# Kernel optimization log

Hardware: AMD Instinct MI355X
Metric: run time of the kernel (lower is better)

The kernel has to match this reference:

```python
import jax, jax.numpy as jnp
import numpy as np

N = 50000      # num nodes
E = 1600000    # num edges
C = 128        # channels
F = 4          # number of framelet filters
K = 6          # Chebyshev order
S = 1.0        # spectral scale s
APPROX = np.array([[0.3, 0.15, 0.1, 0.075, 0.06, 0.05],
                   [0.6, 0.3, 0.2, 0.15, 0.12, 0.1],
                   [0.9, 0.45, 0.3, 0.225, 0.18, 0.15],
                   [1.2, 0.6, 0.4, 0.3, 0.24, 0.2]], dtype=np.float32)


def setup_inputs() -> dict:
    key = jax.random.key(0)
    ks = jax.random.split(key, 6)
    scale = (2.0 / C) ** 0.5
    return {
        "x_real": jax.random.normal(ks[0], (N, C), jnp.float32),
        "x_imag": jax.random.normal(ks[1], (N, C), jnp.float32),
        "edge_index": jax.random.randint(ks[2], (2, E), 0, N, dtype=jnp.int32),
        "edge_weight": jax.random.uniform(ks[3], (E,), jnp.float32),
        "approx": jnp.asarray(APPROX),
        "theta": jnp.ones((F,), jnp.float32),
        "W_r": jax.random.normal(ks[4], (C, C), jnp.float32) * scale,
        "W_i": jax.random.normal(ks[5], (C, C), jnp.float32) * scale,
        "num_nodes": N,
    }


def _framelet_fwd(x_real, x_imag, edge_index, edge_weight, approx, theta, W_r, W_i, num_nodes):
    row, col = edge_index[0], edge_index[1]
    w = edge_weight / S

    def A_norm(h):  # h: [N, C] real; normalized adjacency propagation
        return jax.ops.segment_sum(w[:, None] * h[col], row, num_segments=num_nodes)

    # Linearity: sum_i theta_i * sum_k approx[i,k] * T_k(x) == sum_k c_k * T_k(x)
    c = theta @ approx  # [K] effective Chebyshev coefficients

    T0r, T0i = x_real, x_imag
    out_r = c[0] * T0r
    out_i = c[0] * T0i
    T1r, T1i = -A_norm(T0r), -A_norm(T0i)
    out_r = out_r + c[1] * T1r
    out_i = out_i + c[1] * T1i
    for ki in range(2, K):
        T2r = -2.0 * A_norm(T1r) - T0r
        T2i = -2.0 * A_norm(T1i) - T0i
        out_r = out_r + c[ki] * T2r
        out_i = out_i + c[ki] * T2i
        T0r, T0i, T1r, T1i = T1r, T1i, T2r, T2i

    # complex linear: (r + i*j) @ (W_r + W_i*j)^T
    yr = out_r @ W_r.T - out_i @ W_i.T
    yi = out_r @ W_i.T + out_i @ W_r.T
    # CSiLU: SiLU applied to real/imag parts independently
    return jnp.stack([jax.nn.silu(yr), jax.nn.silu(yi)])  # [2, N, C]


def reference(x_real, x_imag, edge_index, edge_weight, approx, theta, W_r, W_i, num_nodes):
    return _framelet_fwd(x_real, x_imag, edge_index, edge_weight, approx, theta, W_r, W_i, num_nodes)
```

## Files before the change

kernel.cpp:

```cpp
#include <hip/hip_runtime.h>
#include <hip/hip_fp16.h>
#include <math.h>


#define CH   128
#define NP   128
#define NP4  64
#define RPB  128
#define MAXBUCK 512

typedef _Float16 half8 __attribute__((ext_vector_type(8)));
typedef float f32x4 __attribute__((ext_vector_type(4)));

__device__ __forceinline__ uint2 ntload_u2(const uint2* p) {
    unsigned long long v = __builtin_nontemporal_load((const unsigned long long*)p);
    uint2 r; r.x = (unsigned)v; r.y = (unsigned)(v >> 32);
    return r;
}


__global__ __launch_bounds__(256) void bucket_hist_k(
        const int* __restrict__ row, int* __restrict__ bucket_cnt, int E, int nbuck) {
    __shared__ int h[MAXBUCK];
    for (int j = threadIdx.x; j < nbuck; j += 256) h[j] = 0;
    __syncthreads();
    int stride = gridDim.x * 256;
    for (int e = blockIdx.x * 256 + threadIdx.x; e < E; e += stride)
        atomicAdd(&h[row[e] >> 7], 1);
    __syncthreads();
    for (int j = threadIdx.x; j < nbuck; j += 256)
        if (h[j]) atomicAdd(&bucket_cnt[j], h[j]);
}

__global__ __launch_bounds__(512) void bucket_scan_k(
        const int* __restrict__ bucket_cnt, int* __restrict__ bucket_start,
        int* __restrict__ bucket_cursor, int nbuck, int E) {
    __shared__ int sd[MAXBUCK];
    int t = threadIdx.x;
    int v = (t < nbuck) ? bucket_cnt[t] : 0;
    sd[t] = v;
    __syncthreads();
    for (int off = 1; off < MAXBUCK; off <<= 1) {
        int y = (t >= off) ? sd[t - off] : 0;
        __syncthreads();
        sd[t] += y;
        __syncthreads();
    }
    int excl = sd[t] - v;
    if (t < nbuck) { bucket_start[t] = excl; bucket_cursor[t] = excl; }
    if (t == 0) bucket_start[nbuck] = E;
}

__global__ __launch_bounds__(256) void bucket_place_k(
        const int* __restrict__ row, const int* __restrict__ col,
        const float* __restrict__ w, int* __restrict__ bucket_cursor,
        uint2* __restrict__ tmp, int E, int chunk, int nbuck) {
    __shared__ int cnt[MAXBUCK];
    __shared__ int cur[MAXBUCK];
    int e0 = blockIdx.x * chunk;
    int e1 = e0 + chunk; if (e1 > E) e1 = E;
    if (e0 >= E) return;
    for (int j = threadIdx.x; j < nbuck; j += 256) cnt[j] = 0;
    __syncthreads();
    for (int e = e0 + threadIdx.x; e < e1; e += 256)
        atomicAdd(&cnt[row[e] >> 7], 1);
    __syncthreads();
    for (int j = threadIdx.x; j < nbuck; j += 256) {
        int c = cnt[j];
        cur[j] = c ? atomicAdd(&bucket_cursor[j], c) : 0;
    }
    __syncthreads();
    for (int e = e0 + threadIdx.x; e < e1; e += 256) {
        int r = row[e];
        int b = r >> 7;
        int p = atomicAdd(&cur[b], 1);
        uint2 ent;
        ent.x = ((unsigned)(r & (RPB - 1)) << 16) | (unsigned)col[e];
        ent.y = __float_as_uint(w[e]);
        tmp[p] = ent;
    }
}

__global__ __launch_bounds__(256) void csr_build_k(
        const uint2* __restrict__ tmp, const int* __restrict__ bucket_start,
        int* __restrict__ row_start, unsigned* __restrict__ csr4,
        int N, int E, int nbuck) {
    __shared__ int hist[RPB];
    __shared__ int sc[RPB];
    __shared__ int curs[RPB];
    int b = blockIdx.x;
    int t = threadIdx.x;
    int base = bucket_start[b];
    int endp = bucket_start[b + 1];
    if (t < RPB) hist[t] = 0;
    __syncthreads();
    for (int e = base + t; e < endp; e += 256)
        atomicAdd(&hist[tmp[e].x >> 16], 1);
    __syncthreads();
    if (t < RPB) sc[t] = hist[t];
    __syncthreads();
    for (int off = 1; off < RPB; off <<= 1) {
        int y = 0;
        if (t < RPB && t >= off) y = sc[t - off];
        __syncthreads();
        if (t < RPB) sc[t] += y;
        __syncthreads();
    }
    int r0 = b << 7;
    if (t < RPB) {
        int excl = sc[t] - hist[t];
        if (r0 + t < N) row_start[r0 + t] = base + excl;
        curs[t] = base + excl;
    }
    if (b == nbuck - 1 && t == 0) row_start[N] = E;
    __syncthreads();
    for (int e = base + t; e < endp; e += 256) {
        uint2 ent = tmp[e];
        int rl = ent.x >> 16;
        unsigned c = ent.x & 0xffffu;
        float wv = __uint_as_float(ent.y) * (-1.0f / 16.0f);
        int p = atomicAdd(&curs[rl], 1);
        __half hw = __float2half(wv);
        csr4[p] = (c << 16) | (unsigned)__half_as_ushort(hw);
    }
}

__global__ void coef_k(const float* __restrict__ approx, const float* __restrict__ theta,
                       float* cp) {
    int k = threadIdx.x;
    if (k < 6 && blockIdx.x == 0) {
        float s = 0.f;
        for (int f = 0; f < 4; f++) s += theta[f] * approx[f * 6 + k];
        float sc = 1.f;
        for (int j = 0; j < k; j++) sc *= 32.f;
        cp[k] = s * sc;
    }
}

__global__ void convert_x_k(const float2* __restrict__ xr2, const float2* __restrict__ xi2,
                            __half2* __restrict__ xbuf, int total) {
    int idx = blockIdx.x * blockDim.x + threadIdx.x;
    if (idx >= total) return;
    int i = idx >> 7;
    int p = idx & 127;
    float2 v = (p < 64) ? xr2[(size_t)i * 64 + p] : xi2[(size_t)i * 64 + (p - 64)];
    xbuf[idx] = __floats2half2_rn(v.x, v.y);
}

__global__ void build_whT_k(const float* __restrict__ Wr, const float* __restrict__ Wi,
                            _Float16* __restrict__ WhT) {
    int idx = blockIdx.x * 256 + threadIdx.x;
    int j = idx >> 8, k = idx & 255;
    float v;
    if (j < 128) {
        v = (k < 128) ? Wr[j * 128 + k] : -Wi[j * 128 + (k - 128)];
    } else {
        v = (k < 128) ? Wi[(j - 128) * 128 + k] : Wr[(j - 128) * 128 + (k - 128)];
    }
    WhT[idx] = (_Float16)v;
}


__device__ __forceinline__ void unpack4(uint2 v, float& a, float& b, float& c, float& d) {
    __half2 lo = *reinterpret_cast<__half2*>(&v.x);
    __half2 hi = *reinterpret_cast<__half2*>(&v.y);
    float2 f0 = __half22float2(lo);
    float2 f1 = __half22float2(hi);
    a = f0.x; b = f0.y; c = f1.x; d = f1.y;
}

__device__ __forceinline__ void decode(unsigned ent, int& c, float& wv) {
    c = (int)(ent >> 16);
    wv = __half2float(__ushort_as_half((unsigned short)(ent & 0xffffu)));
}

__device__ __forceinline__ void gather_row(
        const uint2* __restrict__ src, const unsigned* __restrict__ csr,
        int beg, int end, int p4,
        float& s0, float& s1, float& s2, float& s3) {
    int e = beg;
    unsigned c0, c1, c2, c3;
    if (e + 4 <= end) { c0 = csr[e]; c1 = csr[e+1]; c2 = csr[e+2]; c3 = csr[e+3]; }
    for (; e + 8 <= end; e += 4) {
        unsigned n0 = csr[e+4], n1 = csr[e+5], n2 = csr[e+6], n3 = csr[e+7];
        int ia, ib, ic, id; float wa, wb, wc, wd;
        decode(c0, ia, wa); decode(c1, ib, wb); decode(c2, ic, wc); decode(c3, id, wd);
        float a0,a1,a2,a3, b0,b1,b2,b3, d0,d1,d2,d3, f0,f1,f2,f3;
        unpack4(src[(size_t)ia * NP4 + p4], a0,a1,a2,a3);
        unpack4(src[(size_t)ib * NP4 + p4], b0,b1,b2,b3);
        unpack4(src[(size_t)ic * NP4 + p4], d0,d1,d2,d3);
        unpack4(src[(size_t)id * NP4 + p4], f0,f1,f2,f3);
        s0 += wa*a0 + wb*b0 + wc*d0 + wd*f0;
        s1 += wa*a1 + wb*b1 + wc*d1 + wd*f1;
        s2 += wa*a2 + wb*b2 + wc*d2 + wd*f2;
        s3 += wa*a3 + wb*b3 + wc*d3 + wd*f3;
        c0 = n0; c1 = n1; c2 = n2; c3 = n3;
    }
    if (e + 4 <= end) {
        int ia, ib, ic, id; float wa, wb, wc, wd;
        decode(c0, ia, wa); decode(c1, ib, wb); decode(c2, ic, wc); decode(c3, id, wd);
        float a0,a1,a2,a3, b0,b1,b2,b3, d0,d1,d2,d3, f0,f1,f2,f3;
        unpack4(src[(size_t)ia * NP4 + p4], a0,a1,a2,a3);
        unpack4(src[(size_t)ib * NP4 + p4], b0,b1,b2,b3);
        unpack4(src[(size_t)ic * NP4 + p4], d0,d1,d2,d3);
        unpack4(src[(size_t)id * NP4 + p4], f0,f1,f2,f3);
        s0 += wa*a0 + wb*b0 + wc*d0 + wd*f0;
        s1 += wa*a1 + wb*b1 + wc*d1 + wd*f1;
        s2 += wa*a2 + wb*b2 + wc*d2 + wd*f2;
        s3 += wa*a3 + wb*b3 + wc*d3 + wd*f3;
        e += 4;
    }
    for (; e < end; e++) {
        int ia; float wa;
        decode(csr[e], ia, wa);
        float a0,a1,a2,a3;
        unpack4(src[(size_t)ia * NP4 + p4], a0,a1,a2,a3);
        s0 += wa*a0; s1 += wa*a1; s2 += wa*a2; s3 += wa*a3;
    }
}

__global__ __launch_bounds__(256) void spmm_first4_k(
        const uint2* __restrict__ xb4,
        const int* __restrict__ row_start, const unsigned* __restrict__ csr,
        uint2* __restrict__ dst, int N) {
    int t = threadIdx.x;
    int rl = t >> 6;
    int p4 = t & 63;
    int i = blockIdx.x * 4 + rl;
    if (i >= N) return;
    int beg = row_start[i], end = row_start[i + 1];
    float s0 = 0.f, s1 = 0.f, s2 = 0.f, s3 = 0.f;
    gather_row(xb4, csr, beg, end, p4, s0, s1, s2, s3);
    s0 *= 0.5f; s1 *= 0.5f; s2 *= 0.5f; s3 *= 0.5f;
    uint2 pk;
    __half2 h0 = __floats2half2_rn(s0, s1);
    __half2 h1 = __floats2half2_rn(s2, s3);
    pk.x = *reinterpret_cast<unsigned*>(&h0);
    pk.y = *reinterpret_cast<unsigned*>(&h1);
    dst[(size_t)i * NP4 + p4] = pk;
}

__global__ __launch_bounds__(256) void spmm_step4_k(
        const uint2* __restrict__ cur, const uint2* __restrict__ prev,
        const int* __restrict__ row_start, const unsigned* __restrict__ csr,
        uint2* __restrict__ dst, int N) {
    int t = threadIdx.x;
    int rl = t >> 6;
    int p4 = t & 63;
    int i = blockIdx.x * 4 + rl;
    if (i >= N) return;
    int beg = row_start[i], end = row_start[i + 1];
    float s0 = 0.f, s1 = 0.f, s2 = 0.f, s3 = 0.f;
    gather_row(cur, csr, beg, end, p4, s0, s1, s2, s3);
    float p0,p1,p2,p3;
    unpack4(ntload_u2(&prev[(size_t)i * NP4 + p4]), p0,p1,p2,p3);
    const float inv = 1.0f / 1024.0f;
    float t0 = s0 - inv * p0;
    float t1v = s1 - inv * p1;
    float t2v = s2 - inv * p2;
    float t3v = s3 - inv * p3;
    uint2 pk;
    __half2 h0 = __floats2half2_rn(t0, t1v);
    __half2 h1 = __floats2half2_rn(t2v, t3v);
    pk.x = *reinterpret_cast<unsigned*>(&h0);
    pk.y = *reinterpret_cast<unsigned*>(&h1);
    dst[(size_t)i * NP4 + p4] = pk;
}

__global__ __launch_bounds__(256) void gemm_silu_mfma_k(
        const _Float16* __restrict__ WhT,
        const uint2* __restrict__ x0, const uint2* __restrict__ t1b,
        const uint2* __restrict__ t2b, const uint2* __restrict__ t3b,
        const float* __restrict__ cp,
        float* __restrict__ out, int N) {
    __shared__ _Float16 U[32][264];
    int t = threadIdx.x;
    int row0 = blockIdx.x * 32;
    const uint2* t4b = (const uint2*)out;
    const uint2* t5b = (const uint2*)out + (size_t)N * NP4;
    const float isc = 1.0f / 32.0f;
    float w0 = cp[0], w1 = cp[1], w2 = cp[2], w3 = cp[3], w4 = cp[4], w5 = cp[5];
    for (int q = t; q < 2048; q += 256) {
        int r = q >> 6;
        int s = q & 63;
        int row = row0 + r;
        float a0 = 0.f, a1 = 0.f, a2 = 0.f, a3 = 0.f;
        if (row < N) {
            size_t idx = (size_t)row * NP4 + s;
            float v0,v1,v2,v3;
            unpack4(ntload_u2(&x0[idx]),  v0,v1,v2,v3);
            a0 += w0*v0; a1 += w0*v1; a2 += w0*v2; a3 += w0*v3;
            unpack4(ntload_u2(&t1b[idx]), v0,v1,v2,v3);
            a0 += w1*v0; a1 += w1*v1; a2 += w1*v2; a3 += w1*v3;
            unpack4(ntload_u2(&t2b[idx]), v0,v1,v2,v3);
            a0 += w2*v0; a1 += w2*v1; a2 += w2*v2; a3 += w2*v3;
            unpack4(ntload_u2(&t3b[idx]), v0,v1,v2,v3);
            a0 += w3*v0; a1 += w3*v1; a2 += w3*v2; a3 += w3*v3;
            unpack4(ntload_u2(&t4b[idx]), v0,v1,v2,v3);
            a0 += w4*v0; a1 += w4*v1; a2 += w4*v2; a3 += w4*v3;
            unpack4(ntload_u2(&t5b[idx]), v0,v1,v2,v3);
            a0 += w5*v0; a1 += w5*v1; a2 += w5*v2; a3 += w5*v3;
        }
        int k = s * 4;
        U[r][k]   = (_Float16)(a0 * isc);
        U[r][k+1] = (_Float16)(a1 * isc);
        U[r][k+2] = (_Float16)(a2 * isc);
        U[r][k+3] = (_Float16)(a3 * isc);
    }
    __syncthreads();

    int wave = t >> 6;
    int lane = t & 63;
    int colbase = wave * 64;
    int lr = lane & 15;
    int lg = lane >> 4;
    f32x4 acc[2][4] = {};
    for (int kb = 0; kb < 8; kb++) {
        int k0 = kb * 32 + lg * 8;
        half8 a0 = *(const half8*)&U[lr][k0];
        half8 a1 = *(const half8*)&U[16 + lr][k0];
        #pragma unroll
        for (int nf = 0; nf < 4; nf++) {
            int col = colbase + nf * 16 + lr;
            half8 b = *(const half8*)&WhT[(size_t)col * 256 + k0];
            acc[0][nf] = __builtin_amdgcn_mfma_f32_16x16x32_f16(a0, b, acc[0][nf], 0, 0, 0);
            acc[1][nf] = __builtin_amdgcn_mfma_f32_16x16x32_f16(a1, b, acc[1][nf], 0, 0, 0);
        }
    }

    #pragma unroll
    for (int mf = 0; mf < 2; mf++) {
        #pragma unroll
        for (int nf = 0; nf < 4; nf++) {
            int col = colbase + nf * 16 + lr;
            int half = col >> 7, j = col & 127;
            #pragma unroll
            for (int r4 = 0; r4 < 4; r4++) {
                int row = row0 + mf * 16 + lg * 4 + r4;
                if (row < N) {
                    float v = acc[mf][nf][r4] * 32.f;
                    float sv = v / (1.f + expf(-v));
                    out[(size_t)half * N * CH + (size_t)row * CH + j] = sv;
                }
            }
        }
    }
}


extern "C" void kernel_launch(void* const* d_in, const int* in_sizes, int n_in,
                              void* d_out, int out_size, void* d_ws, size_t ws_size,
                              hipStream_t stream) {
    const float* xr     = (const float*)d_in[0];
    const float* xi     = (const float*)d_in[1];
    const int*   eidx   = (const int*)d_in[2];
    const float* ew     = (const float*)d_in[3];
    const float* approx = (const float*)d_in[4];
    const float* theta  = (const float*)d_in[5];
    const float* Wr     = (const float*)d_in[6];
    const float* Wi     = (const float*)d_in[7];

    const int N = in_sizes[0] / CH;
    const int E = in_sizes[3];
    const int* rowv = eidx;
    const int* colv = eidx + E;

    float* outp = (float*)d_out;

    char* w8 = (char*)d_ws;
    size_t off = 0;
    auto alloc = [&](size_t bytes) -> void* {
        void* ptr = w8 + off;
        off += (bytes + 255) & ~(size_t)255;
        return ptr;
    };
    float*    cp        = (float*)alloc(64 * 4);
    int*      bucket_cnt= (int*)alloc(MAXBUCK * 4);
    int*      bucket_st = (int*)alloc((MAXBUCK + 1) * 4);
    int*      bucket_cur= (int*)alloc(MAXBUCK * 4);
    int*      row_start = (int*)alloc((size_t)(N + 1) * 4);
    unsigned* csr4      = (unsigned*)alloc((size_t)E * 4);
    _Float16* WhT       = (_Float16*)alloc(256 * 256 * 2);
    uint2*    xbuf      = (uint2*)alloc((size_t)N * NP4 * 8);
    uint2*    T1        = (uint2*)alloc((size_t)N * NP4 * 8);
    uint2*    T2        = (uint2*)alloc((size_t)N * NP4 * 8);
    uint2*    T3        = (uint2*)alloc((size_t)N * NP4 * 8);
    uint2*    tmp       = T3;
    uint2*    T4        = (uint2*)d_out;
    uint2*    T5        = (uint2*)d_out + (size_t)N * NP4;
    (void)ws_size;

    const int nbuck = (N + RPB - 1) / RPB;
    const int chunk = (E + 255) / 256;
    const int NH = N * NP;

    hipMemsetAsync(bucket_cnt, 0, (size_t)MAXBUCK * 4, stream);
    coef_k<<<1, 64, 0, stream>>>(approx, theta, cp);
    build_whT_k<<<256, 256, 0, stream>>>(Wr, Wi, WhT);
    bucket_hist_k<<<256, 256, 0, stream>>>(rowv, bucket_cnt, E, nbuck);
    bucket_scan_k<<<1, MAXBUCK, 0, stream>>>(bucket_cnt, bucket_st, bucket_cur, nbuck, E);
    bucket_place_k<<<256, 256, 0, stream>>>(rowv, colv, ew, bucket_cur, tmp, E, chunk, nbuck);
    csr_build_k<<<nbuck, 256, 0, stream>>>(tmp, bucket_st, row_start, csr4, N, E, nbuck);
    convert_x_k<<<(NH + 255) / 256, 256, 0, stream>>>(
        (const float2*)xr, (const float2*)xi, (__half2*)xbuf, NH);

    const int NG = (N + 3) / 4;

    spmm_first4_k<<<NG, 256, 0, stream>>>(xbuf, row_start, csr4, T1, N);
    spmm_step4_k<<<NG, 256, 0, stream>>>(T1, xbuf, row_start, csr4, T2, N);
    spmm_step4_k<<<NG, 256, 0, stream>>>(T2, T1, row_start, csr4, T3, N);
    spmm_step4_k<<<NG, 256, 0, stream>>>(T3, T2, row_start, csr4, T4, N);
    spmm_step4_k<<<NG, 256, 0, stream>>>(T4, T3, row_start, csr4, T5, N);

    gemm_silu_mfma_k<<<(N + 31) / 32, 256, 0, stream>>>(
        WhT, xbuf, T1, T2, T3, cp, outp, N);
}
```

Baseline: 658.8 us.

## Tile feature layout into 8-channel-chunk blocks and degree-sort row pairs for SpMM

Feature buffers now use a blocked layout in which each 8-row group stores 64-byte column chunks contiguously. The SpMM grid is split into 8 channel slices per block, so each gather touches a narrower slice that is more likely to stay in cache. Rows are processed in pairs sorted by max degree through a histogram, scan and scatter, which balances the per-wave work, and outputs use nontemporal stores. This adds three preprocessing kernels and sorted-index indirection. Because N/2 pairs only cover 2*(N/2) rows, an odd N would leave the last row unhandled.

Result: slower. 743.3 us (+12.8%).

```diff
diff --git a/kernel.cpp b/kernel.cpp
--- a/kernel.cpp
+++ b/kernel.cpp
@@ -4,8 +4,6 @@
 
 
 #define CH   128
-#define NP   128
-#define NP4  64
 #define RPB  128
 #define MAXBUCK 512
 
@@ -16,6 +14,14 @@
     unsigned long long v = __builtin_nontemporal_load((const unsigned long long*)p);
     uint2 r; r.x = (unsigned)v; r.y = (unsigned)(v >> 32);
     return r;
+}
+__device__ __forceinline__ void ntstore_u2(uint2* p, uint2 v) {
+    unsigned long long q = (unsigned long long)v.x | ((unsigned long long)v.y << 32);
+    __builtin_nontemporal_store(q, (unsigned long long*)p);
+}
+
+__device__ __forceinline__ size_t foff(int i, int cbase ) {
+    return ((size_t)((unsigned)i >> 3) << 9) + (((unsigned)i & 7u) << 3) + cbase;
 }
 
 
@@ -125,6 +131,54 @@
     }
 }
 
+
+__global__ __launch_bounds__(256) void pair_hist_k(
+        const int* __restrict__ row_start, int* __restrict__ ph, int NP_) {
+    __shared__ int h[256];
+    if (threadIdx.x < 256) h[threadIdx.x] = 0;
+    __syncthreads();
+    int stride = gridDim.x * 256;
+    for (int i = blockIdx.x * 256 + threadIdx.x; i < NP_; i += stride) {
+        int a = row_start[2*i], b = row_start[2*i+1], c = row_start[2*i+2];
+        int d = max(b - a, c - b);
+        if (d > 255) d = 255;
+        atomicAdd(&h[d], 1);
+    }
+    __syncthreads();
+    if (threadIdx.x < 256 && h[threadIdx.x]) atomicAdd(&ph[threadIdx.x], h[threadIdx.x]);
+}
+
+__global__ __launch_bounds__(256) void pair_scan_k(
+        const int* __restrict__ ph, int* __restrict__ pcur) {
+    __shared__ int sd[256];
+    int t = threadIdx.x;
+    int v = ph[t];
+    sd[t] = v;
+    __syncthreads();
+    for (int off = 1; off < 256; off <<= 1) {
+        int y = (t >= off) ? sd[t - off] : 0;
+        __syncthreads();
+        sd[t] += y;
+        __syncthreads();
+    }
+    pcur[t] = sd[t] - v;
+}
+
+__global__ __launch_bounds__(256) void pair_scatter_k(
+        const int* __restrict__ row_start, int* __restrict__ pcur,
+        int* __restrict__ sbeg, int* __restrict__ send, int* __restrict__ sorig,
+        int NP_) {
+    int i = blockIdx.x * 256 + threadIdx.x;
+    if (i >= NP_) return;
+    int a = row_start[2*i], b = row_start[2*i+1], c = row_start[2*i+2];
+    int d = max(b - a, c - b);
+    if (d > 255) d = 255;
+    int q = atomicAdd(&pcur[d], 1);
+    int p = 2 * q;
+    sbeg[p]   = a; send[p]   = b; sorig[p]   = 2*i;
+    sbeg[p+1] = b; send[p+1] = c; sorig[p+1] = 2*i + 1;
+}
+
 __global__ void coef_k(const float* __restrict__ approx, const float* __restrict__ theta,
                        float* cp) {
     int k = threadIdx.x;
@@ -137,14 +191,22 @@
     }
 }
 
-__global__ void convert_x_k(const float2* __restrict__ xr2, const float2* __restrict__ xi2,
-                            __half2* __restrict__ xbuf, int total) {
+__global__ void convert_x_k(const float4* __restrict__ xr4, const float4* __restrict__ xi4,
+                            uint2* __restrict__ xbuf, int N) {
     int idx = blockIdx.x * blockDim.x + threadIdx.x;
-    if (idx >= total) return;
-    int i = idx >> 7;
-    int p = idx & 127;
-    float2 v = (p < 64) ? xr2[(size_t)i * 64 + p] : xi2[(size_t)i * 64 + (p - 64)];
-    xbuf[idx] = __floats2half2_rn(v.x, v.y);
+    if (idx >= N * 64) return;
+    int i = idx >> 6;
+    int sq = idx & 63;
+    int h = sq * 4;
+    int fl = h & 127;
+    float4 v = (h < 128) ? xr4[(size_t)i * 32 + (fl >> 2)] : xi4[(size_t)i * 32 + (fl >> 2)];
+    __half2 h0 = __floats2half2_rn(v.x, v.y);
+    __half2 h1 = __floats2half2_rn(v.z, v.w);
+    uint2 pk;
+    pk.x = *reinterpret_cast<unsigned*>(&h0);
+    pk.y = *reinterpret_cast<unsigned*>(&h1);
+    int c = sq >> 3, s = sq & 7;
+    xbuf[foff(i, c * 64 + s)] = pk;
 }
 
 __global__ void build_whT_k(const float* __restrict__ Wr, const float* __restrict__ Wi,
@@ -169,102 +231,86 @@
     a = f0.x; b = f0.y; c = f1.x; d = f1.y;
 }
 
-__device__ __forceinline__ void decode(unsigned ent, int& c, float& wv) {
-    c = (int)(ent >> 16);
-    wv = __half2float(__ushort_as_half((unsigned short)(ent & 0xffffu)));
-}
-
-__device__ __forceinline__ void gather_row(
-        const uint2* __restrict__ src, const unsigned* __restrict__ csr,
-        int beg, int end, int p4,
-        float& s0, float& s1, float& s2, float& s3) {
+#define GFMA(ENT)                                                              \
+    {                                                                          \
+        int col = (int)((ENT) >> 16);                                          \
+        float w = __half2float(__ushort_as_half((unsigned short)((ENT) & 0xffffu))); \
+        uint2 v = cur[foff(col, cbase)];                                       \
+        float a0,a1,a2,a3;                                                     \
+        unpack4(v, a0,a1,a2,a3);                                               \
+        s0 += w*a0; s1 += w*a1; s2 += w*a2; s3 += w*a3;                        \
+    }
+
+__global__ __launch_bounds__(256) void spmm_first8_k(
+        const uint2* __restrict__ cur, const unsigned* __restrict__ csr,
+        const int* __restrict__ sbeg, const int* __restrict__ send,
+        const int* __restrict__ sorig, uint2* __restrict__ dst, int N) {
+    int c = blockIdx.x & 7;
+    int rb = blockIdx.x >> 3;
+    int lane = threadIdx.x & 63, wave = threadIdx.x >> 6;
+    int j = lane >> 3, s = lane & 7;
+    int p = rb * 32 + wave * 8 + j;
+    if (p >= N) return;
+    int beg = sbeg[p], end = send[p], orig = sorig[p];
+    int cbase = c * 64 + s;
+    float s0 = 0.f, s1 = 0.f, s2 = 0.f, s3 = 0.f;
     int e = beg;
-    unsigned c0, c1, c2, c3;
-    if (e + 4 <= end) { c0 = csr[e]; c1 = csr[e+1]; c2 = csr[e+2]; c3 = csr[e+3]; }
-    for (; e + 8 <= end; e += 4) {
-        unsigned n0 = csr[e+4], n1 = csr[e+5], n2 = csr[e+6], n3 = csr[e+7];
-        int ia, ib, ic, id; float wa, wb, wc, wd;
-        decode(c0, ia, wa); decode(c1, ib, wb); decode(c2, ic, wc); decode(c3, id, wd);
-        float a0,a1,a2,a3, b0,b1,b2,b3, d0,d1,d2,d3, f0,f1,f2,f3;
-        unpack4(src[(size_t)ia * NP4 + p4], a0,a1,a2,a3);
-        unpack4(src[(size_t)ib * NP4 + p4], b0,b1,b2,b3);
-        unpack4(src[(size_t)ic * NP4 + p4], d0,d1,d2,d3);
-        unpack4(src[(size_t)id * NP4 + p4], f0,f1,f2,f3);
-        s0 += wa*a0 + wb*b0 + wc*d0 + wd*f0;
-        s1 += wa*a1 + wb*b1 + wc*d1 + wd*f1;
-        s2 += wa*a2 + wb*b2 + wc*d2 + wd*f2;
-        s3 += wa*a3 + wb*b3 + wc*d3 + wd*f3;
-        c0 = n0; c1 = n1; c2 = n2; c3 = n3;
-    }
-    if (e + 4 <= end) {
-        int ia, ib, ic, id; float wa, wb, wc, wd;
-        decode(c0, ia, wa); decode(c1, ib, wb); decode(c2, ic, wc); decode(c3, id, wd);
-        float a0,a1,a2,a3, b0,b1,b2,b3, d0,d1,d2,d3, f0,f1,f2,f3;
-        unpack4(src[(size_t)ia * NP4 + p4], a0,a1,a2,a3);
-        unpack4(src[(size_t)ib * NP4 + p4], b0,b1,b2,b3);
-        unpack4(src[(size_t)ic * NP4 + p4], d0,d1,d2,d3);
-        unpack4(src[(size_t)id * NP4 + p4], f0,f1,f2,f3);
-        s0 += wa*a0 + wb*b0 + wc*d0 + wd*f0;
-        s1 += wa*a1 + wb*b1 + wc*d1 + wd*f1;
-        s2 += wa*a2 + wb*b2 + wc*d2 + wd*f2;
-        s3 += wa*a3 + wb*b3 + wc*d3 + wd*f3;
-        e += 4;
-    }
-    for (; e < end; e++) {
-        int ia; float wa;
-        decode(csr[e], ia, wa);
-        float a0,a1,a2,a3;
-        unpack4(src[(size_t)ia * NP4 + p4], a0,a1,a2,a3);
-        s0 += wa*a0; s1 += wa*a1; s2 += wa*a2; s3 += wa*a3;
-    }
-}
-
-__global__ __launch_bounds__(256) void spmm_first4_k(
-        const uint2* __restrict__ xb4,
-        const int* __restrict__ row_start, const unsigned* __restrict__ csr,
-        uint2* __restrict__ dst, int N) {
-    int t = threadIdx.x;
-    int rl = t >> 6;
-    int p4 = t & 63;
-    int i = blockIdx.x * 4 + rl;
-    if (i >= N) return;
-    int beg = row_start[i], end = row_start[i + 1];
-    float s0 = 0.f, s1 = 0.f, s2 = 0.f, s3 = 0.f;
-    gather_row(xb4, csr, beg, end, p4, s0, s1, s2, s3);
+    unsigned ea, eb;
+    if (e + 2 <= end) { ea = csr[e]; eb = csr[e+1]; }
+    for (; e + 4 <= end; e += 2) {
+        unsigned na = csr[e+2], nb = csr[e+3];
+        GFMA(ea); GFMA(eb);
+        ea = na; eb = nb;
+    }
+    if (e + 2 <= end) { GFMA(ea); GFMA(eb); e += 2; }
+    for (; e < end; e++) { unsigned ent = csr[e]; GFMA(ent); }
     s0 *= 0.5f; s1 *= 0.5f; s2 *= 0.5f; s3 *= 0.5f;
-    uint2 pk;
     __half2 h0 = __floats2half2_rn(s0, s1);
     __half2 h1 = __floats2half2_rn(s2, s3);
+    uint2 pk;
     pk.x = *reinterpret_cast<unsigned*>(&h0);
     pk.y = *reinterpret_cast<unsigned*>(&h1);
-    dst[(size_t)i * NP4 + p4] = pk;
-}
-
-__global__ __launch_bounds__(256) void spmm_step4_k(
+    ntstore_u2(&dst[foff(orig, cbase)], pk);
+}
+
+__global__ __launch_bounds__(256) void spmm_step8_k(
         const uint2* __restrict__ cur, const uint2* __restrict__ prev,
-        const int* __restrict__ row_start, const unsigned* __restrict__ csr,
-        uint2* __restrict__ dst, int N) {
-    int t = threadIdx.x;
-    int rl = t >> 6;
-    int p4 = t & 63;
-    int i = blockIdx.x * 4 + rl;
-    if (i >= N) return;
-    int beg = row_start[i], end = row_start[i + 1];
+        const unsigned* __restrict__ csr,
+        const int* __restrict__ sbeg, const int* __restrict__ send,
+        const int* __restrict__ sorig, uint2* __restrict__ dst, int N) {
+    int c = blockIdx.x & 7;
+    int rb = blockIdx.x >> 3;
+    int lane = threadIdx.x & 63, wave = threadIdx.x >> 6;
+    int j = lane >> 3, s = lane & 7;
+    int p = rb * 32 + wave * 8 + j;
+    if (p >= N) return;
+    int beg = sbeg[p], end = send[p], orig = sorig[p];
+    int cbase = c * 64 + s;
     float s0 = 0.f, s1 = 0.f, s2 = 0.f, s3 = 0.f;
-    gather_row(cur, csr, beg, end, p4, s0, s1, s2, s3);
+    int e = beg;
+    unsigned ea, eb;
+    if (e + 2 <= end) { ea = csr[e]; eb = csr[e+1]; }
+    for (; e + 4 <= end; e += 2) {
+        unsigned na = csr[e+2], nb = csr[e+3];
+        GFMA(ea); GFMA(eb);
+        ea = na; eb = nb;
+    }
+    if (e + 2 <= end) { GFMA(ea); GFMA(eb); e += 2; }
+    for (; e < end; e++) { unsigned ent = csr[e]; GFMA(ent); }
+    size_t po = foff(orig, cbase);
     float p0,p1,p2,p3;
-    unpack4(ntload_u2(&prev[(size_t)i * NP4 + p4]), p0,p1,p2,p3);
+    unpack4(ntload_u2(&prev[po]), p0,p1,p2,p3);
     const float inv = 1.0f / 1024.0f;
     float t0 = s0 - inv * p0;
     float t1v = s1 - inv * p1;
     float t2v = s2 - inv * p2;
     float t3v = s3 - inv * p3;
-    uint2 pk;
     __half2 h0 = __floats2half2_rn(t0, t1v);
     __half2 h1 = __floats2half2_rn(t2v, t3v);
+    uint2 pk;
     pk.x = *reinterpret_cast<unsigned*>(&h0);
     pk.y = *reinterpret_cast<unsigned*>(&h1);
-    dst[(size_t)i * NP4 + p4] = pk;
+    ntstore_u2(&dst[po], pk);
 }
 
 __global__ __launch_bounds__(256) void gemm_silu_mfma_k(
@@ -277,16 +323,16 @@
     int t = threadIdx.x;
     int row0 = blockIdx.x * 32;
     const uint2* t4b = (const uint2*)out;
-    const uint2* t5b = (const uint2*)out + (size_t)N * NP4;
+    const uint2* t5b = (const uint2*)out + (size_t)N * 64;
     const float isc = 1.0f / 32.0f;
     float w0 = cp[0], w1 = cp[1], w2 = cp[2], w3 = cp[3], w4 = cp[4], w5 = cp[5];
     for (int q = t; q < 2048; q += 256) {
         int r = q >> 6;
-        int s = q & 63;
+        int sq = q & 63;
         int row = row0 + r;
         float a0 = 0.f, a1 = 0.f, a2 = 0.f, a3 = 0.f;
         if (row < N) {
-            size_t idx = (size_t)row * NP4 + s;
+            size_t idx = foff(row, (sq >> 3) * 64 + (sq & 7));
             float v0,v1,v2,v3;
             unpack4(ntload_u2(&x0[idx]),  v0,v1,v2,v3);
             a0 += w0*v0; a1 += w0*v1; a2 += w0*v2; a3 += w0*v3;
@@ -301,7 +347,7 @@
             unpack4(ntload_u2(&t5b[idx]), v0,v1,v2,v3);
             a0 += w5*v0; a1 += w5*v1; a2 += w5*v2; a3 += w5*v3;
         }
-        int k = s * 4;
+        int k = sq * 4;
         U[r][k]   = (_Float16)(a0 * isc);
         U[r][k+1] = (_Float16)(a1 * isc);
         U[r][k+2] = (_Float16)(a2 * isc);
@@ -333,14 +379,14 @@
         #pragma unroll
         for (int nf = 0; nf < 4; nf++) {
             int col = colbase + nf * 16 + lr;
-            int half = col >> 7, j = col & 127;
+            int half = col >> 7, jj = col & 127;
             #pragma unroll
             for (int r4 = 0; r4 < 4; r4++) {
                 int row = row0 + mf * 16 + lg * 4 + r4;
                 if (row < N) {
                     float v = acc[mf][nf][r4] * 32.f;
                     float sv = v / (1.f + expf(-v));
-                    out[(size_t)half * N * CH + (size_t)row * CH + j] = sv;
+                    out[(size_t)half * N * CH + (size_t)row * CH + jj] = sv;
                 }
             }
         }
@@ -378,39 +424,49 @@
     int*      bucket_cnt= (int*)alloc(MAXBUCK * 4);
     int*      bucket_st = (int*)alloc((MAXBUCK + 1) * 4);
     int*      bucket_cur= (int*)alloc(MAXBUCK * 4);
+    int*      ph        = (int*)alloc(256 * 4);
+    int*      pcur      = (int*)alloc(256 * 4);
     int*      row_start = (int*)alloc((size_t)(N + 1) * 4);
+    int*      sbeg      = (int*)alloc((size_t)N * 4);
+    int*      send      = (int*)alloc((size_t)N * 4);
+    int*      sorig     = (int*)alloc((size_t)N * 4);
     unsigned* csr4      = (unsigned*)alloc((size_t)E * 4);
     _Float16* WhT       = (_Float16*)alloc(256 * 256 * 2);
-    uint2*    xbuf      = (uint2*)alloc((size_t)N * NP4 * 8);
-    uint2*    T1        = (uint2*)alloc((size_t)N * NP4 * 8);
-    uint2*    T2        = (uint2*)alloc((size_t)N * NP4 * 8);
-    uint2*    T3        = (uint2*)alloc((size_t)N * NP4 * 8);
+    uint2*    xbuf      = (uint2*)alloc((size_t)N * 64 * 8);
+    uint2*    T1        = (uint2*)alloc((size_t)N * 64 * 8);
+    uint2*    T2        = (uint2*)alloc((size_t)N * 64 * 8);
+    uint2*    T3        = (uint2*)alloc((size_t)N * 64 * 8);
     uint2*    tmp       = T3;
     uint2*    T4        = (uint2*)d_out;
-    uint2*    T5        = (uint2*)d_out + (size_t)N * NP4;
+    uint2*    T5        = (uint2*)d_out + (size_t)N * 64;
     (void)ws_size;
 
     const int nbuck = (N + RPB - 1) / RPB;
     const int chunk = (E + 255) / 256;
-    const int NH = N * NP;
+    const int NPairs = N / 2;
 
     hipMemsetAsync(bucket_cnt, 0, (size_t)MAXBUCK * 4, stream);
+    hipMemsetAsync(ph, 0, 256 * 4, stream);
     coef_k<<<1, 64, 0, stream>>>(approx, theta, cp);
     build_whT_k<<<256, 256, 0, stream>>>(Wr, Wi, WhT);
     bucket_hist_k<<<256, 256, 0, stream>>>(rowv, bucket_cnt, E, nbuck);
     bucket_scan_k<<<1, MAXBUCK, 0, stream>>>(bucket_cnt, bucket_st, bucket_cur, nbuck, E);
     bucket_place_k<<<256, 256, 0, stream>>>(rowv, colv, ew, bucket_cur, tmp, E, chunk, nbuck);
     csr_build_k<<<nbuck, 256, 0, stream>>>(tmp, bucket_st, row_start, csr4, N, E, nbuck);
-    convert_x_k<<<(NH + 255) / 256, 256, 0, stream>>>(
-        (const float2*)xr, (const float2*)xi, (__half2*)xbuf, NH);
-
-    const int NG = (N + 3) / 4;
-
-    spmm_first4_k<<<NG, 256, 0, stream>>>(xbuf, row_start, csr4, T1, N);
-    spmm_step4_k<<<NG, 256, 0, stream>>>(T1, xbuf, row_start, csr4, T2, N);
-    spmm_step4_k<<<NG, 256, 0, stream>>>(T2, T1, row_start, csr4, T3, N);
-    spmm_step4_k<<<NG, 256, 0, stream>>>(T3, T2, row_start, csr4, T4, N);
-    spmm_step4_k<<<NG, 256, 0, stream>>>(T4, T3, row_start, csr4, T5, N);
+    pair_hist_k<<<128, 256, 0, stream>>>(row_start, ph, NPairs);
+    pair_scan_k<<<1, 256, 0, stream>>>(ph, pcur);
+    pair_scatter_k<<<(NPairs + 255) / 256, 256, 0, stream>>>(
+        row_start, pcur, sbeg, send, sorig, NPairs);
+    convert_x_k<<<(N * 64 + 255) / 256, 256, 0, stream>>>(
+        (const float4*)xr, (const float4*)xi, xbuf, N);
+
+    const int NG = 8 * ((N + 31) / 32);
+
+    spmm_first8_k<<<NG, 256, 0, stream>>>(xbuf, csr4, sbeg, send, sorig, T1, N);
+    spmm_step8_k<<<NG, 256, 0, stream>>>(T1, xbuf, csr4, sbeg, send, sorig, T2, N);
+    spmm_step8_k<<<NG, 256, 0, stream>>>(T2, T1, csr4, sbeg, send, sorig, T3, N);
+    spmm_step8_k<<<NG, 256, 0, stream>>>(T3, T2, csr4, sbeg, send, sorig, T4, N);
+    spmm_step8_k<<<NG, 256, 0, stream>>>(T4, T3, csr4, sbeg, send, sorig, T5, N);
 
     gemm_silu_mfma_k<<<(N + 31) / 32, 256, 0, stream>>>(
         WhT, xbuf, T1, T2, T3, cp, outp, N);
```
